# Performance work log

Hardware: AMD Instinct MI355X
Metric: run time of the kernel (lower is better)

## Reference

```python
import jax, jax.numpy as jnp
import numpy as np

B, S, D = 2, 2048, 2048
KVH, QPG, HD = 8, 4, 64          # kv heads, q heads per group, head size
THETA = 1024.0
PARTIAL = 0.5
SOFT_CAP = 50.0
EPS = 1e-5


def setup_inputs() -> dict:
    key = jax.random.key(0)
    ks = jax.random.split(key, 8)
    scale = 0.02
    return {
        "x": jax.random.normal(ks[0], (B, S, D), jnp.float32),
        "wq": jax.random.normal(ks[1], (KVH, QPG, HD, D), jnp.float32) * scale,
        "wk": jax.random.normal(ks[2], (KVH, HD, D), jnp.float32) * scale,
        "wv": jax.random.normal(ks[3], (KVH, HD, D), jnp.float32) * scale,
        "wo": jax.random.normal(ks[4], (D, KVH, QPG, HD), jnp.float32) * scale,
        "qn_w": jnp.ones((HD,), jnp.float32),
        "kn_w": jnp.ones((HD,), jnp.float32),
        "pos_ids": jnp.arange(S, dtype=jnp.int32),
    }


def _rms_norm(t, w):
    var = jnp.mean(jnp.square(t), axis=-1, keepdims=True)
    return t * jax.lax.rsqrt(var + EPS) * w


def _rope_tables(pos_ids):
    half = HD // 2
    rotated_size = int(HD * PARTIAL)
    inv_freq = 1.0 / THETA ** (jnp.arange(0, 2 * half, 2, dtype=jnp.float32) / rotated_size)
    inv_freq = jnp.where(jnp.arange(half) < rotated_size // 2, inv_freq, 0.0)
    freqs = pos_ids.astype(jnp.float32)[:, None] * inv_freq[None, :]   # [S, half]
    emb = jnp.concatenate([freqs, freqs], axis=-1)                      # [S, HD]
    return jnp.cos(emb), jnp.sin(emb)


def _apply_rope(t, cos, sin):
    # t: [..., S, HD]; rotate_half: (x1, x2) -> (-x2, x1)
    half = HD // 2
    x1, x2 = t[..., :half], t[..., half:]
    rot = jnp.concatenate([-x2, x1], axis=-1)
    return t * cos + rot * sin


def reference(x, wq, wk, wv, wo, qn_w, kn_w, pos_ids):
    # QKV projections (GQA)
    q = jnp.einsum("bsd,gphd->bgpsh", x, wq)   # [B,KVH,QPG,S,HD]
    k = jnp.einsum("bsd,ghd->bgsh", x, wk)      # [B,KVH,S,HD]
    v = jnp.einsum("bsd,ghd->bgsh", x, wv)

    # QK-norm (RMS over head dim)
    q = _rms_norm(q, qn_w)
    k = _rms_norm(k, kn_w)

    # partial RoPE
    cos, sin = _rope_tables(pos_ids)            # [S, HD]
    q = _apply_rope(q, cos, sin).astype(x.dtype)
    k = _apply_rope(k, cos, sin).astype(x.dtype)

    # attention in fp32 (upcast_attn) with soft cap and causal mask
    scale = 1.0 / jnp.sqrt(jnp.float32(HD))
    scores = jnp.einsum("bgpsh,bgth->bgpst", q.astype(jnp.float32), k.astype(jnp.float32)) * scale
    scores = SOFT_CAP * jnp.tanh(scores / SOFT_CAP)
    causal = pos_ids[:, None] >= pos_ids[None, :]                    # [S, S]
    scores = jnp.where(causal, scores, jnp.finfo(jnp.float32).min)
    probs = jax.nn.softmax(scores, axis=-1)
    attn = jnp.einsum("bgpst,bgth->bgpsh", probs, v.astype(jnp.float32)).astype(x.dtype)

    # output projection (flatten kv_head x q_heads_per_group -> heads)
    out = jnp.einsum("bgpsh,dgph->bsd", attn, wo)
    return out
```

## Files before the change

kernel.cpp:

```cpp
#include <hip/hip_runtime.h>
#include <stdint.h>

#define S_LEN   2048
#define D_MODEL 2048
#define N_KVH   8
#define N_QPG   4
#define N_HD    64

typedef __attribute__((ext_vector_type(8))) short  short8;
typedef __attribute__((ext_vector_type(4))) short  short4v;
typedef __attribute__((ext_vector_type(4))) float  float4v;

__device__ __forceinline__ unsigned short f2bf(float x) {
    unsigned int u = __float_as_uint(x);
    u = (u + 0x7fffu + ((u >> 16) & 1u)) >> 16;
    return (unsigned short)u;
}

__device__ __forceinline__ void gload_lds16(const unsigned short* g, unsigned short* l) {
    __builtin_amdgcn_global_load_lds((const __attribute__((address_space(1))) unsigned int*)g,
                                     (__attribute__((address_space(3))) unsigned int*)l,
                                     16, 0, 0);
}

__device__ __forceinline__ short8 lds_read8(const unsigned short* p) {
    union { short8 s8; short4v s4[2]; } u;
    u.s4[0] = *(const short4v*)p;
    u.s4[1] = *(const short4v*)(p + 4);
    return u.s8;
}

__global__ __launch_bounds__(256) void cvt_all(const float* __restrict__ x,
                                               const float* __restrict__ wq,
                                               const float* __restrict__ wk,
                                               const float* __restrict__ wv,
                                               const float* __restrict__ wo,
                                               unsigned short* __restrict__ xb,
                                               unsigned short* __restrict__ wqb,
                                               unsigned short* __restrict__ wkb,
                                               unsigned short* __restrict__ wvb,
                                               unsigned short* __restrict__ wob) {
    size_t i = (size_t)blockIdx.x * 256 + threadIdx.x;
    const float* src; unsigned short* dst; size_t off;
    if      (i < 1048576) { src = x;  dst = xb;  off = i; }
    else if (i < 1572864) { src = wq; dst = wqb; off = i - 1048576; }
    else if (i < 1703936) { src = wk; dst = wkb; off = i - 1572864; }
    else if (i < 1835008) { src = wv; dst = wvb; off = i - 1703936; }
    else                  { src = wo; dst = wob; off = i - 1835008; }
    const float4* p = (const float4*)src + off * 2;
    float4 a = p[0], b = p[1];
    union { unsigned short us[8]; uint4 v; } u;
    u.us[0] = f2bf(a.x); u.us[1] = f2bf(a.y); u.us[2] = f2bf(a.z); u.us[3] = f2bf(a.w);
    u.us[4] = f2bf(b.x); u.us[5] = f2bf(b.y); u.us[6] = f2bf(b.z); u.us[7] = f2bf(b.w);
    ((uint4*)dst)[off] = u.v;
}

#define EPI_OUT 0
#define EPI_Q   1
#define EPI_K   2
#define EPI_V   3

template<int EPI>
__global__ __launch_bounds__(256)
void gemm_bt(const unsigned short* __restrict__ A,
             const unsigned short* __restrict__ B,
             void* __restrict__ C,
             const float* __restrict__ normw,
             int M, int N, int K)
{
    __shared__ __align__(16) unsigned short Alds[128 * 32];
    __shared__ __align__(16) unsigned short Blds[128 * 32];

    const int tid  = threadIdx.x;
    const int lane = tid & 63;
    const int wave = tid >> 6;
    const int quad = lane >> 4;
    const int l15  = lane & 15;
    const int m0 = blockIdx.x * 128;
    const int n0 = blockIdx.y * 128;
    const int wm = (wave >> 1) * 64;
    const int wn = (wave & 1) * 64;

    float4v acc[4][4];
#pragma unroll
    for (int i = 0; i < 4; i++)
#pragma unroll
        for (int j = 0; j < 4; j++) acc[i][j] = (float4v){0.f, 0.f, 0.f, 0.f};

    const int j0 = wave * 2;
    const int lr = lane >> 2;
    const int lc = (lane & 3) * 8;
    const unsigned short* Ag = A + (size_t)(m0 + j0 * 16 + lr) * K + lc;
    const unsigned short* Bg = B + (size_t)(n0 + j0 * 16 + lr) * K + lc;
    unsigned short* Al = Alds + j0 * 512;
    unsigned short* Bl = Blds + j0 * 512;

    for (int k0 = 0; k0 < K; k0 += 32) {
        __syncthreads();
        gload_lds16(Ag + k0,          Al);
        gload_lds16(Ag + 16 * K + k0, Al + 512);
        gload_lds16(Bg + k0,          Bl);
        gload_lds16(Bg + 16 * K + k0, Bl + 512);
        __syncthreads();

        short8 af[4], bf[4];
#pragma unroll
        for (int mt = 0; mt < 4; mt++)
            af[mt] = *(const short8*)(Alds + (wm + mt * 16 + l15) * 32 + quad * 8);
#pragma unroll
        for (int nt = 0; nt < 4; nt++)
            bf[nt] = *(const short8*)(Blds + (wn + nt * 16 + l15) * 32 + quad * 8);
#pragma unroll
        for (int mt = 0; mt < 4; mt++)
#pragma unroll
            for (int nt = 0; nt < 4; nt++)
                acc[mt][nt] = __builtin_amdgcn_mfma_f32_16x16x32_bf16(af[mt], bf[nt], acc[mt][nt], 0, 0, 0);
    }

    const int nb = n0 + wn;
#pragma unroll
    for (int mt = 0; mt < 4; mt++) {
#pragma unroll
        for (int r = 0; r < 4; r++) {
            const int m = m0 + wm + mt * 16 + quad * 4 + r;
            if constexpr (EPI == EPI_OUT) {
#pragma unroll
                for (int nt = 0; nt < 4; nt++) {
                    int n = nb + nt * 16 + l15;
                    ((float*)C)[(size_t)m * N + n] = acc[mt][nt][r];
                }
            } else if constexpr (EPI == EPI_V) {
                const int bidx = m >> 11, s = m & 2047;
#pragma unroll
                for (int nt = 0; nt < 4; nt++) {
                    int n = nb + nt * 16 + l15;
                    int g = n >> 6, h = n & 63;
                    ((unsigned short*)C)[((size_t)(bidx * N_KVH + g) * S_LEN + s) * N_HD + h] =
                        f2bf(acc[mt][nt][r]);
                }
            } else {
                float v0 = acc[mt][0][r], v1 = acc[mt][1][r], v2 = acc[mt][2][r], v3 = acc[mt][3][r];
                float s2 = v0 * v0 + v1 * v1 + v2 * v2 + v3 * v3;
#pragma unroll
                for (int off = 1; off < 16; off <<= 1) s2 += __shfl_xor(s2, off, 64);
                float rs = rsqrtf(s2 * (1.0f / 64.0f) + 1e-5f);
                float nv0 = v0 * rs * normw[0 * 16 + l15];
                float nv1 = v1 * rs * normw[1 * 16 + l15];
                float nv2 = v2 * rs * normw[2 * 16 + l15];
                float nv3 = v3 * rs * normw[3 * 16 + l15];
                const int bidx = m >> 11, s = m & 2047;
                float ang = (float)s * exp2f(-0.625f * (float)l15);
                float sn, cs;
                __sincosf(ang, &sn, &cs);
                float o0 = nv0 * cs - nv2 * sn;
                float o2 = nv2 * cs + nv0 * sn;
                float o1 = nv1, o3 = nv3;
                unsigned short* dst;
                if constexpr (EPI == EPI_Q) {
                    const int g = nb >> 8, p = (nb >> 6) & 3;
                    dst = (unsigned short*)C +
                        ((((size_t)bidx * N_KVH + g) * N_QPG + p) * S_LEN + s) * N_HD;
                } else {
                    const int g = nb >> 6;
                    dst = (unsigned short*)C +
                        (((size_t)bidx * N_KVH + g) * S_LEN + s) * N_HD;
                }
                dst[0 * 16 + l15] = f2bf(o0);
                dst[1 * 16 + l15] = f2bf(o1);
                dst[2 * 16 + l15] = f2bf(o2);
                dst[3 * 16 + l15] = f2bf(o3);
            }
        }
    }
}

#define KSTRIDE 68
#define PSTRIDE 68

__global__ __launch_bounds__(256)
void attn_kernel(const unsigned short* __restrict__ Q,
                 const unsigned short* __restrict__ Kb,
                 const unsigned short* __restrict__ V,
                 unsigned short* __restrict__ O)
{
    __shared__ __align__(16) unsigned short Klds[64 * KSTRIDE];
    __shared__ __align__(16) unsigned short Vt[64 * KSTRIDE];
    __shared__ __align__(16) unsigned short Plds[4 * 32 * PSTRIDE];

    const int tid  = threadIdx.x;
    const int lane = tid & 63;
    const int w    = tid >> 6;
    const int quad = lane >> 4;
    const int l15  = lane & 15;
    const int qx = blockIdx.x;
    const int bg = blockIdx.y;
    const int b = bg >> 3, g = bg & 7;

    const unsigned short* qbase = Q + (((size_t)b * N_KVH + g) * N_QPG + w) * S_LEN * N_HD;
    const unsigned short* kbase = Kb + ((size_t)b * N_KVH + g) * S_LEN * N_HD;
    const unsigned short* vbase = V + ((size_t)b * N_KVH + g) * S_LEN * N_HD;

    unsigned short* Pw = Plds + w * (32 * PSTRIDE);

    for (int half = 0; half < 2; half++) {
        const int qt = half ? (63 - qx) : qx;
        const int qrow0 = qt * 32;

        short8 qf[2][2];
#pragma unroll
        for (int mt = 0; mt < 2; mt++)
#pragma unroll
            for (int ks = 0; ks < 2; ks++)
                qf[mt][ks] = *(const short8*)(qbase + (size_t)(qrow0 + mt * 16 + l15) * N_HD + ks * 32 + quad * 8);

        float4v o_acc[2][4];
#pragma unroll
        for (int mt = 0; mt < 2; mt++)
#pragma unroll
            for (int nt = 0; nt < 4; nt++) o_acc[mt][nt] = (float4v){0.f, 0.f, 0.f, 0.f};
        float rsum[2][4];
#pragma unroll
        for (int mt = 0; mt < 2; mt++)
#pragma unroll
            for (int r = 0; r < 4; r++) rsum[mt][r] = 0.f;

        const int ktmax = (qrow0 + 31) >> 6;
        for (int kt = 0; kt <= ktmax; kt++) {
            __syncthreads();
            {
                const unsigned short* kb = kbase + (size_t)(kt * 64) * N_HD;
                int r = tid >> 2, c = (tid & 3) * 16;
                uint4 k0 = *(const uint4*)(kb + r * 64 + c);
                uint4 k1 = *(const uint4*)(kb + r * 64 + c + 8);
                unsigned short* kd = Klds + r * KSTRIDE + c;
                *(uint2*)(kd)      = make_uint2(k0.x, k0.y);
                *(uint2*)(kd + 4)  = make_uint2(k0.z, k0.w);
                *(uint2*)(kd + 8)  = make_uint2(k1.x, k1.y);
                *(uint2*)(kd + 12) = make_uint2(k1.z, k1.w);
                const unsigned short* vb = vbase + (size_t)(kt * 64) * N_HD;
                int vr = tid & 63, h0 = (tid >> 6) * 16;
                uint4 va  = *(const uint4*)(vb + vr * 64 + h0);
                uint4 vb2 = *(const uint4*)(vb + vr * 64 + h0 + 8);
                const unsigned short* pa = (const unsigned short*)&va;
                const unsigned short* pb = (const unsigned short*)&vb2;
#pragma unroll
                for (int j = 0; j < 8; j++) Vt[(h0 + j) * KSTRIDE + vr] = pa[j];
#pragma unroll
                for (int j = 0; j < 8; j++) Vt[(h0 + 8 + j) * KSTRIDE + vr] = pb[j];
            }
            __syncthreads();

            float4v s_acc[2][4];
#pragma unroll
            for (int mt = 0; mt < 2; mt++)
#pragma unroll
                for (int nt = 0; nt < 4; nt++) s_acc[mt][nt] = (float4v){0.f, 0.f, 0.f, 0.f};
#pragma unroll
            for (int ks = 0; ks < 2; ks++) {
                short8 kf[4];
#pragma unroll
                for (int nt = 0; nt < 4; nt++)
                    kf[nt] = lds_read8(Klds + (nt * 16 + l15) * KSTRIDE + ks * 32 + quad * 8);
#pragma unroll
                for (int mt = 0; mt < 2; mt++)
#pragma unroll
                    for (int nt = 0; nt < 4; nt++)
                        s_acc[mt][nt] = __builtin_amdgcn_mfma_f32_16x16x32_bf16(qf[mt][ks], kf[nt], s_acc[mt][nt], 0, 0, 0);
            }

#pragma unroll
            for (int mt = 0; mt < 2; mt++) {
#pragma unroll
                for (int r = 0; r < 4; r++) {
                    const int s_q = qrow0 + mt * 16 + quad * 4 + r;
                    const int prow = (mt * 16 + quad * 4 + r) * PSTRIDE;
#pragma unroll
                    for (int nt = 0; nt < 4; nt++) {
                        float t = __expf(s_acc[mt][nt][r] * 0.005f);
                        float p = __expf(-100.0f * __builtin_amdgcn_rcpf(t + 1.0f));
                        int s_k = kt * 64 + nt * 16 + l15;
                        p = (s_k <= s_q) ? p : 0.0f;
                        unsigned short pbits = f2bf(p);
                        Pw[prow + nt * 16 + l15] = pbits;
                        rsum[mt][r] += __uint_as_float((unsigned)pbits << 16);
                    }
                }
            }

#pragma unroll
            for (int ks = 0; ks < 2; ks++) {
                short8 pf[2], vf[4];
#pragma unroll
                for (int mt = 0; mt < 2; mt++)
                    pf[mt] = lds_read8(Pw + (mt * 16 + l15) * PSTRIDE + ks * 32 + quad * 8);
#pragma unroll
                for (int nt = 0; nt < 4; nt++)
                    vf[nt] = lds_read8(Vt + (nt * 16 + l15) * KSTRIDE + ks * 32 + quad * 8);
#pragma unroll
                for (int mt = 0; mt < 2; mt++)
#pragma unroll
                    for (int nt = 0; nt < 4; nt++)
                        o_acc[mt][nt] = __builtin_amdgcn_mfma_f32_16x16x32_bf16(pf[mt], vf[nt], o_acc[mt][nt], 0, 0, 0);
            }
        }

#pragma unroll
        for (int mt = 0; mt < 2; mt++) {
#pragma unroll
            for (int r = 0; r < 4; r++) {
                float s = rsum[mt][r];
                s += __shfl_xor(s, 1, 64);
                s += __shfl_xor(s, 2, 64);
                s += __shfl_xor(s, 4, 64);
                s += __shfl_xor(s, 8, 64);
                float inv = 1.0f / s;
                int s_q = qrow0 + mt * 16 + quad * 4 + r;
                size_t rowoff = ((size_t)(b * S_LEN + s_q)) * D_MODEL + (g * N_QPG + w) * N_HD;
#pragma unroll
                for (int nt = 0; nt < 4; nt++)
                    O[rowoff + nt * 16 + l15] = f2bf(o_acc[mt][nt][r] * inv);
            }
        }
    }
}

extern "C" void kernel_launch(void* const* d_in, const int* in_sizes, int n_in,
                              void* d_out, int out_size, void* d_ws, size_t ws_size,
                              hipStream_t stream)
{
    const float* x    = (const float*)d_in[0];
    const float* wq   = (const float*)d_in[1];
    const float* wk   = (const float*)d_in[2];
    const float* wv   = (const float*)d_in[3];
    const float* wo   = (const float*)d_in[4];
    const float* qn_w = (const float*)d_in[5];
    const float* kn_w = (const float*)d_in[6];

    char* ws = (char*)d_ws;
    unsigned short* xb  = (unsigned short*)(ws + 0);
    unsigned short* wqb = (unsigned short*)(ws + 16777216);
    unsigned short* wkb = (unsigned short*)(ws + 25165824);
    unsigned short* wvb = (unsigned short*)(ws + 27262976);
    unsigned short* wob = (unsigned short*)(ws + 29360128);
    unsigned short* qb  = (unsigned short*)(ws + 37748736);
    unsigned short* kb  = (unsigned short*)(ws + 54525952);
    unsigned short* vb  = (unsigned short*)(ws + 58720256);
    unsigned short* ab  = (unsigned short*)(ws + 62914560);

    cvt_all<<<dim3(9216), 256, 0, stream>>>(x, wq, wk, wv, wo, xb, wqb, wkb, wvb, wob);

    gemm_bt<EPI_Q><<<dim3(32, 16), 256, 0, stream>>>(xb, wqb, qb, qn_w, 4096, 2048, 2048);
    gemm_bt<EPI_K><<<dim3(32, 4),  256, 0, stream>>>(xb, wkb, kb, kn_w, 4096, 512, 2048);
    gemm_bt<EPI_V><<<dim3(32, 4),  256, 0, stream>>>(xb, wvb, vb, nullptr, 4096, 512, 2048);

    attn_kernel<<<dim3(32, 16), 256, 0, stream>>>(qb, kb, vb, ab);

    gemm_bt<EPI_OUT><<<dim3(32, 16), 256, 0, stream>>>(ab, wob, d_out, nullptr, 4096, 2048, 2048);
}
```

Baseline: 432.1 us.

## Fuse K/V projections, emit transposed V, and restructure attention tiles

K and V projections are merged into one launch, with the V half computed as Wv·xᵀ so that V is written already transposed per head. The attention kernel then loads K and Vᵀ straight into fragment-ordered LDS with global_load_lds, which drops the per-tile register transpose and padded LDS stores. The kernel also launches one q-tile per block (64x16 grid, heaviest tiles first) instead of pairing tiles, sets a min-blocks launch bound, applies the causal mask only on the diagonal tile, and replaces the tanh soft-cap exp chain with a polynomial approximation. Risks: the transposed V writes are strided and uncoalesced, and the polynomial tanh is only accurate for small scores.

```diff
diff --git a/kernel.cpp b/kernel.cpp
--- a/kernel.cpp
+++ b/kernel.cpp
@@ -57,8 +57,6 @@
 
 #define EPI_OUT 0
 #define EPI_Q   1
-#define EPI_K   2
-#define EPI_V   3
 
 template<int EPI>
 __global__ __launch_bounds__(256)
@@ -128,15 +126,6 @@
                 for (int nt = 0; nt < 4; nt++) {
                     int n = nb + nt * 16 + l15;
                     ((float*)C)[(size_t)m * N + n] = acc[mt][nt][r];
-                }
-            } else if constexpr (EPI == EPI_V) {
-                const int bidx = m >> 11, s = m & 2047;
-#pragma unroll
-                for (int nt = 0; nt < 4; nt++) {
-                    int n = nb + nt * 16 + l15;
-                    int g = n >> 6, h = n & 63;
-                    ((unsigned short*)C)[((size_t)(bidx * N_KVH + g) * S_LEN + s) * N_HD + h] =
-                        f2bf(acc[mt][nt][r]);
                 }
             } else {
                 float v0 = acc[mt][0][r], v1 = acc[mt][1][r], v2 = acc[mt][2][r], v3 = acc[mt][3][r];
@@ -154,37 +143,131 @@
                 __sincosf(ang, &sn, &cs);
                 float o0 = nv0 * cs - nv2 * sn;
                 float o2 = nv2 * cs + nv0 * sn;
-                float o1 = nv1, o3 = nv3;
-                unsigned short* dst;
-                if constexpr (EPI == EPI_Q) {
-                    const int g = nb >> 8, p = (nb >> 6) & 3;
-                    dst = (unsigned short*)C +
-                        ((((size_t)bidx * N_KVH + g) * N_QPG + p) * S_LEN + s) * N_HD;
-                } else {
-                    const int g = nb >> 6;
-                    dst = (unsigned short*)C +
-                        (((size_t)bidx * N_KVH + g) * S_LEN + s) * N_HD;
+                const int g = nb >> 8, p = (nb >> 6) & 3;
+                unsigned short* dst = (unsigned short*)C +
+                    ((((size_t)bidx * N_KVH + g) * N_QPG + p) * S_LEN + s) * N_HD;
+                dst[0 * 16 + l15] = f2bf(o0);
+                dst[1 * 16 + l15] = f2bf(nv1);
+                dst[2 * 16 + l15] = f2bf(o2);
+                dst[3 * 16 + l15] = f2bf(nv3);
+            }
+        }
+    }
+}
+
+__global__ __launch_bounds__(256)
+void gemm_kv(const unsigned short* __restrict__ xb,
+             const unsigned short* __restrict__ wkb,
+             const unsigned short* __restrict__ wvb,
+             unsigned short* __restrict__ kout,
+             unsigned short* __restrict__ vtout,
+             const float* __restrict__ knw)
+{
+    __shared__ __align__(16) unsigned short Alds[128 * 32];
+    __shared__ __align__(16) unsigned short Blds[128 * 32];
+
+    const int tid  = threadIdx.x;
+    const int lane = tid & 63;
+    const int wave = tid >> 6;
+    const int quad = lane >> 4;
+    const int l15  = lane & 15;
+    const int bx = blockIdx.x, by = blockIdx.y;
+    const bool isK = (by < 4);
+    const unsigned short* A = isK ? xb  : wvb;
+    const unsigned short* B = isK ? wkb : xb;
+    const int m0 = isK ? bx * 128 : (by - 4) * 128;
+    const int n0 = isK ? by * 128 : bx * 128;
+    const int K = 2048;
+    const int wm = (wave >> 1) * 64;
+    const int wn = (wave & 1) * 64;
+
+    float4v acc[4][4];
+#pragma unroll
+    for (int i = 0; i < 4; i++)
+#pragma unroll
+        for (int j = 0; j < 4; j++) acc[i][j] = (float4v){0.f, 0.f, 0.f, 0.f};
+
+    const int j0 = wave * 2;
+    const int lr = lane >> 2;
+    const int lc = (lane & 3) * 8;
+    const unsigned short* Ag = A + (size_t)(m0 + j0 * 16 + lr) * K + lc;
+    const unsigned short* Bg = B + (size_t)(n0 + j0 * 16 + lr) * K + lc;
+    unsigned short* Al = Alds + j0 * 512;
+    unsigned short* Bl = Blds + j0 * 512;
+
+    for (int k0 = 0; k0 < K; k0 += 32) {
+        __syncthreads();
+        gload_lds16(Ag + k0,          Al);
+        gload_lds16(Ag + 16 * K + k0, Al + 512);
+        gload_lds16(Bg + k0,          Bl);
+        gload_lds16(Bg + 16 * K + k0, Bl + 512);
+        __syncthreads();
+
+        short8 af[4], bf[4];
+#pragma unroll
+        for (int mt = 0; mt < 4; mt++)
+            af[mt] = *(const short8*)(Alds + (wm + mt * 16 + l15) * 32 + quad * 8);
+#pragma unroll
+        for (int nt = 0; nt < 4; nt++)
+            bf[nt] = *(const short8*)(Blds + (wn + nt * 16 + l15) * 32 + quad * 8);
+#pragma unroll
+        for (int mt = 0; mt < 4; mt++)
+#pragma unroll
+            for (int nt = 0; nt < 4; nt++)
+                acc[mt][nt] = __builtin_amdgcn_mfma_f32_16x16x32_bf16(af[mt], bf[nt], acc[mt][nt], 0, 0, 0);
+    }
+
+    const int nb = n0 + wn;
+#pragma unroll
+    for (int mt = 0; mt < 4; mt++) {
+#pragma unroll
+        for (int r = 0; r < 4; r++) {
+            const int m = m0 + wm + mt * 16 + quad * 4 + r;
+            if (isK) {
+                float v0 = acc[mt][0][r], v1 = acc[mt][1][r], v2 = acc[mt][2][r], v3 = acc[mt][3][r];
+                float s2 = v0 * v0 + v1 * v1 + v2 * v2 + v3 * v3;
+#pragma unroll
+                for (int off = 1; off < 16; off <<= 1) s2 += __shfl_xor(s2, off, 64);
+                float rs = rsqrtf(s2 * (1.0f / 64.0f) + 1e-5f);
+                float nv0 = v0 * rs * knw[0 * 16 + l15];
+                float nv1 = v1 * rs * knw[1 * 16 + l15];
+                float nv2 = v2 * rs * knw[2 * 16 + l15];
+                float nv3 = v3 * rs * knw[3 * 16 + l15];
+                const int bidx = m >> 11, s = m & 2047;
+                float ang = (float)s * exp2f(-0.625f * (float)l15);
+                float sn, cs;
+                __sincosf(ang, &sn, &cs);
+                float o0 = nv0 * cs - nv2 * sn;
+                float o2 = nv2 * cs + nv0 * sn;
+                const int g = nb >> 6;
+                unsigned short* dst = kout +
+                    (((size_t)bidx * N_KVH + g) * S_LEN + s) * N_HD;
+                dst[0 * 16 + l15] = f2bf(o0);
+                dst[1 * 16 + l15] = f2bf(nv1);
+                dst[2 * 16 + l15] = f2bf(o2);
+                dst[3 * 16 + l15] = f2bf(nv3);
+            } else {
+#pragma unroll
+                for (int nt = 0; nt < 4; nt++) {
+                    int n = nb + nt * 16 + l15;
+                    vtout[((size_t)(n >> 11) * 512 + m) * 2048 + (n & 2047)] =
+                        f2bf(acc[mt][nt][r]);
                 }
-                dst[0 * 16 + l15] = f2bf(o0);
-                dst[1 * 16 + l15] = f2bf(o1);
-                dst[2 * 16 + l15] = f2bf(o2);
-                dst[3 * 16 + l15] = f2bf(o3);
             }
         }
     }
 }
 
-#define KSTRIDE 68
 #define PSTRIDE 68
 
-__global__ __launch_bounds__(256)
+__global__ __launch_bounds__(256, 4)
 void attn_kernel(const unsigned short* __restrict__ Q,
                  const unsigned short* __restrict__ Kb,
-                 const unsigned short* __restrict__ V,
+                 const unsigned short* __restrict__ Vt,
                  unsigned short* __restrict__ O)
 {
-    __shared__ __align__(16) unsigned short Klds[64 * KSTRIDE];
-    __shared__ __align__(16) unsigned short Vt[64 * KSTRIDE];
+    __shared__ __align__(16) unsigned short Kf[8 * 512];
+    __shared__ __align__(16) unsigned short Vf[8 * 512];
     __shared__ __align__(16) unsigned short Plds[4 * 32 * PSTRIDE];
 
     const int tid  = threadIdx.x;
@@ -192,134 +275,139 @@
     const int w    = tid >> 6;
     const int quad = lane >> 4;
     const int l15  = lane & 15;
-    const int qx = blockIdx.x;
+    const int lhi  = lane >> 4;
+    const int qt = 63 - blockIdx.x;
+    const int qrow0 = qt * 32;
     const int bg = blockIdx.y;
     const int b = bg >> 3, g = bg & 7;
 
-    const unsigned short* qbase = Q + (((size_t)b * N_KVH + g) * N_QPG + w) * S_LEN * N_HD;
-    const unsigned short* kbase = Kb + ((size_t)b * N_KVH + g) * S_LEN * N_HD;
-    const unsigned short* vbase = V + ((size_t)b * N_KVH + g) * S_LEN * N_HD;
+    const unsigned short* qbase  = Q  + (((size_t)b * N_KVH + g) * N_QPG + w) * S_LEN * N_HD;
+    const unsigned short* kbase  = Kb + ((size_t)b * N_KVH + g) * S_LEN * N_HD;
+    const unsigned short* vtbase = Vt + ((size_t)b * N_KVH + g) * (size_t)N_HD * S_LEN;
+
+    const unsigned short* sptr[4];
+    unsigned short*       ldst[4];
+    int                   step[4];
+#pragma unroll
+    for (int j = 0; j < 4; j++) {
+        int ri = w * 4 + j;
+        int isV = ri >> 3, rr = ri & 7, nt = rr >> 1, ks = rr & 1;
+        if (isV) {
+            sptr[j] = vtbase + (size_t)(nt * 16 + l15) * S_LEN + ks * 32 + lhi * 8;
+            step[j] = 64;
+            ldst[j] = Vf + rr * 512;
+        } else {
+            sptr[j] = kbase + (size_t)(nt * 16 + l15) * N_HD + ks * 32 + lhi * 8;
+            step[j] = 64 * N_HD;
+            ldst[j] = Kf + rr * 512;
+        }
+    }
 
     unsigned short* Pw = Plds + w * (32 * PSTRIDE);
 
-    for (int half = 0; half < 2; half++) {
-        const int qt = half ? (63 - qx) : qx;
-        const int qrow0 = qt * 32;
-
-        short8 qf[2][2];
+    short8 qf[2][2];
+#pragma unroll
+    for (int mt = 0; mt < 2; mt++)
+#pragma unroll
+        for (int ks = 0; ks < 2; ks++)
+            qf[mt][ks] = *(const short8*)(qbase + (size_t)(qrow0 + mt * 16 + l15) * N_HD + ks * 32 + quad * 8);
+
+    float4v o_acc[2][4];
+#pragma unroll
+    for (int mt = 0; mt < 2; mt++)
+#pragma unroll
+        for (int nt = 0; nt < 4; nt++) o_acc[mt][nt] = (float4v){0.f, 0.f, 0.f, 0.f};
+    float rsum[2][4];
+#pragma unroll
+    for (int mt = 0; mt < 2; mt++)
+#pragma unroll
+        for (int r = 0; r < 4; r++) rsum[mt][r] = 0.f;
+
+    const int ktend = qrow0 >> 6;
+    for (int kt = 0; kt <= ktend; kt++) {
+        __syncthreads();
+#pragma unroll
+        for (int j = 0; j < 4; j++)
+            gload_lds16(sptr[j] + (size_t)kt * step[j], ldst[j]);
+        __syncthreads();
+
+        float4v s_acc[2][4];
 #pragma unroll
         for (int mt = 0; mt < 2; mt++)
 #pragma unroll
-            for (int ks = 0; ks < 2; ks++)
-                qf[mt][ks] = *(const short8*)(qbase + (size_t)(qrow0 + mt * 16 + l15) * N_HD + ks * 32 + quad * 8);
-
-        float4v o_acc[2][4];
-#pragma unroll
-        for (int mt = 0; mt < 2; mt++)
-#pragma unroll
-            for (int nt = 0; nt < 4; nt++) o_acc[mt][nt] = (float4v){0.f, 0.f, 0.f, 0.f};
-        float rsum[2][4];
-#pragma unroll
-        for (int mt = 0; mt < 2; mt++)
-#pragma unroll
-            for (int r = 0; r < 4; r++) rsum[mt][r] = 0.f;
-
-        const int ktmax = (qrow0 + 31) >> 6;
-        for (int kt = 0; kt <= ktmax; kt++) {
-            __syncthreads();
-            {
-                const unsigned short* kb = kbase + (size_t)(kt * 64) * N_HD;
-                int r = tid >> 2, c = (tid & 3) * 16;
-                uint4 k0 = *(const uint4*)(kb + r * 64 + c);
-                uint4 k1 = *(const uint4*)(kb + r * 64 + c + 8);
-                unsigned short* kd = Klds + r * KSTRIDE + c;
-                *(uint2*)(kd)      = make_uint2(k0.x, k0.y);
-                *(uint2*)(kd + 4)  = make_uint2(k0.z, k0.w);
-                *(uint2*)(kd + 8)  = make_uint2(k1.x, k1.y);
-                *(uint2*)(kd + 12) = make_uint2(k1.z, k1.w);
-                const unsigned short* vb = vbase + (size_t)(kt * 64) * N_HD;
-                int vr = tid & 63, h0 = (tid >> 6) * 16;
-                uint4 va  = *(const uint4*)(vb + vr * 64 + h0);
-                uint4 vb2 = *(const uint4*)(vb + vr * 64 + h0 + 8);
-                const unsigned short* pa = (const unsigned short*)&va;
-                const unsigned short* pb = (const unsigned short*)&vb2;
-#pragma unroll
-                for (int j = 0; j < 8; j++) Vt[(h0 + j) * KSTRIDE + vr] = pa[j];
-#pragma unroll
-                for (int j = 0; j < 8; j++) Vt[(h0 + 8 + j) * KSTRIDE + vr] = pb[j];
-            }
-            __syncthreads();
-
-            float4v s_acc[2][4];
+            for (int nt = 0; nt < 4; nt++) s_acc[mt][nt] = (float4v){0.f, 0.f, 0.f, 0.f};
+#pragma unroll
+        for (int ks = 0; ks < 2; ks++) {
+            short8 kfr[4];
+#pragma unroll
+            for (int nt = 0; nt < 4; nt++)
+                kfr[nt] = *(const short8*)(Kf + (nt * 2 + ks) * 512 + lane * 8);
 #pragma unroll
             for (int mt = 0; mt < 2; mt++)
 #pragma unroll
-                for (int nt = 0; nt < 4; nt++) s_acc[mt][nt] = (float4v){0.f, 0.f, 0.f, 0.f};
-#pragma unroll
-            for (int ks = 0; ks < 2; ks++) {
-                short8 kf[4];
-#pragma unroll
                 for (int nt = 0; nt < 4; nt++)
-                    kf[nt] = lds_read8(Klds + (nt * 16 + l15) * KSTRIDE + ks * 32 + quad * 8);
-#pragma unroll
-                for (int mt = 0; mt < 2; mt++)
-#pragma unroll
-                    for (int nt = 0; nt < 4; nt++)
-                        s_acc[mt][nt] = __builtin_amdgcn_mfma_f32_16x16x32_bf16(qf[mt][ks], kf[nt], s_acc[mt][nt], 0, 0, 0);
-            }
-
-#pragma unroll
-            for (int mt = 0; mt < 2; mt++) {
-#pragma unroll
-                for (int r = 0; r < 4; r++) {
-                    const int s_q = qrow0 + mt * 16 + quad * 4 + r;
-                    const int prow = (mt * 16 + quad * 4 + r) * PSTRIDE;
-#pragma unroll
-                    for (int nt = 0; nt < 4; nt++) {
-                        float t = __expf(s_acc[mt][nt][r] * 0.005f);
-                        float p = __expf(-100.0f * __builtin_amdgcn_rcpf(t + 1.0f));
+                    s_acc[mt][nt] = __builtin_amdgcn_mfma_f32_16x16x32_bf16(qf[mt][ks], kfr[nt], s_acc[mt][nt], 0, 0, 0);
+        }
+
+        const bool diag = (kt == ktend);
+#pragma unroll
+        for (int mt = 0; mt < 2; mt++) {
+#pragma unroll
+            for (int r = 0; r < 4; r++) {
+                const int s_q  = qrow0 + mt * 16 + quad * 4 + r;
+                const int prow = (mt * 16 + quad * 4 + r) * PSTRIDE;
+#pragma unroll
+                for (int nt = 0; nt < 4; nt++) {
+                    float a = s_acc[mt][nt][r];
+                    float z = a * 2.5e-3f;
+                    float u = z * z;
+                    float t1 = fmaf(u, 0.13333334f, -0.33333334f);
+                    float t2 = fmaf(u, t1, 1.0f);
+                    float sc = a * 0.125f * t2;
+                    float p = __builtin_amdgcn_exp2f(fmaf(sc, 1.44269504f, -72.13475204f));
+                    if (diag) {
                         int s_k = kt * 64 + nt * 16 + l15;
                         p = (s_k <= s_q) ? p : 0.0f;
-                        unsigned short pbits = f2bf(p);
-                        Pw[prow + nt * 16 + l15] = pbits;
-                        rsum[mt][r] += __uint_as_float((unsigned)pbits << 16);
                     }
+                    unsigned short pb = f2bf(p);
+                    Pw[prow + nt * 16 + l15] = pb;
+                    rsum[mt][r] += __uint_as_float((unsigned)pb << 16);
                 }
             }
-
-#pragma unroll
-            for (int ks = 0; ks < 2; ks++) {
-                short8 pf[2], vf[4];
-#pragma unroll
-                for (int mt = 0; mt < 2; mt++)
-                    pf[mt] = lds_read8(Pw + (mt * 16 + l15) * PSTRIDE + ks * 32 + quad * 8);
+        }
+
+#pragma unroll
+        for (int ks = 0; ks < 2; ks++) {
+            short8 pf[2], vfr[4];
+#pragma unroll
+            for (int mt = 0; mt < 2; mt++)
+                pf[mt] = lds_read8(Pw + (mt * 16 + l15) * PSTRIDE + ks * 32 + quad * 8);
+#pragma unroll
+            for (int nt = 0; nt < 4; nt++)
+                vfr[nt] = *(const short8*)(Vf + (nt * 2 + ks) * 512 + lane * 8);
+#pragma unroll
+            for (int mt = 0; mt < 2; mt++)
 #pragma unroll
                 for (int nt = 0; nt < 4; nt++)
-                    vf[nt] = lds_read8(Vt + (nt * 16 + l15) * KSTRIDE + ks * 32 + quad * 8);
-#pragma unroll
-                for (int mt = 0; mt < 2; mt++)
-#pragma unroll
-                    for (int nt = 0; nt < 4; nt++)
-                        o_acc[mt][nt] = __builtin_amdgcn_mfma_f32_16x16x32_bf16(pf[mt], vf[nt], o_acc[mt][nt], 0, 0, 0);
-            }
-        }
-
-#pragma unroll
-        for (int mt = 0; mt < 2; mt++) {
-#pragma unroll
-            for (int r = 0; r < 4; r++) {
-                float s = rsum[mt][r];
-                s += __shfl_xor(s, 1, 64);
-                s += __shfl_xor(s, 2, 64);
-                s += __shfl_xor(s, 4, 64);
-                s += __shfl_xor(s, 8, 64);
-                float inv = 1.0f / s;
-                int s_q = qrow0 + mt * 16 + quad * 4 + r;
-                size_t rowoff = ((size_t)(b * S_LEN + s_q)) * D_MODEL + (g * N_QPG + w) * N_HD;
-#pragma unroll
-                for (int nt = 0; nt < 4; nt++)
-                    O[rowoff + nt * 16 + l15] = f2bf(o_acc[mt][nt][r] * inv);
-            }
+                    o_acc[mt][nt] = __builtin_amdgcn_mfma_f32_16x16x32_bf16(pf[mt], vfr[nt], o_acc[mt][nt], 0, 0, 0);
+        }
+    }
+
+#pragma unroll
+    for (int mt = 0; mt < 2; mt++) {
+#pragma unroll
+        for (int r = 0; r < 4; r++) {
+            float s = rsum[mt][r];
+            s += __shfl_xor(s, 1, 64);
+            s += __shfl_xor(s, 2, 64);
+            s += __shfl_xor(s, 4, 64);
+            s += __shfl_xor(s, 8, 64);
+            float inv = 1.0f / s;
+            int s_q = qrow0 + mt * 16 + quad * 4 + r;
+            size_t rowoff = ((size_t)(b * S_LEN + s_q)) * D_MODEL + (g * N_QPG + w) * N_HD;
+#pragma unroll
+            for (int nt = 0; nt < 4; nt++)
+                O[rowoff + nt * 16 + l15] = f2bf(o_acc[mt][nt][r] * inv);
         }
     }
 }
@@ -344,16 +432,15 @@
     unsigned short* wob = (unsigned short*)(ws + 29360128);
     unsigned short* qb  = (unsigned short*)(ws + 37748736);
     unsigned short* kb  = (unsigned short*)(ws + 54525952);
-    unsigned short* vb  = (unsigned short*)(ws + 58720256);
+    unsigned short* vt  = (unsigned short*)(ws + 58720256);
     unsigned short* ab  = (unsigned short*)(ws + 62914560);
 
     cvt_all<<<dim3(9216), 256, 0, stream>>>(x, wq, wk, wv, wo, xb, wqb, wkb, wvb, wob);
 
     gemm_bt<EPI_Q><<<dim3(32, 16), 256, 0, stream>>>(xb, wqb, qb, qn_w, 4096, 2048, 2048);
-    gemm_bt<EPI_K><<<dim3(32, 4),  256, 0, stream>>>(xb, wkb, kb, kn_w, 4096, 512, 2048);
-    gemm_bt<EPI_V><<<dim3(32, 4),  256, 0, stream>>>(xb, wvb, vb, nullptr, 4096, 512, 2048);
-
-    attn_kernel<<<dim3(32, 16), 256, 0, stream>>>(qb, kb, vb, ab);
+    gemm_kv<<<dim3(32, 8), 256, 0, stream>>>(xb, wkb, wvb, kb, vt, kn_w);
+
+    attn_kernel<<<dim3(64, 16), 256, 0, stream>>>(qb, kb, vt, ab);
 
     gemm_bt<EPI_OUT><<<dim3(32, 16), 256, 0, stream>>>(ab, wob, d_out, nullptr, 4096, 2048, 2048);
 }
```

New measurement: 430.2 us. About the same (-0.4%).
